# Performance work log

Hardware: AMD Instinct MI355X
Metric: run time of the kernel (lower is better)

The kernel has to match this reference:

```python
import jax, jax.numpy as jnp
import numpy as np

B, S, D = 4, 2048, 768
H = 12
HD = D // H  # 64


def setup_inputs() -> dict:
    key = jax.random.key(0)
    k1, k2, k3 = jax.random.split(key, 3)
    return {
        "hidden_states": jax.random.normal(k1, (B, S, D), dtype=jnp.float32),
        "W_attn": jax.random.normal(k2, (D, 3 * D), dtype=jnp.float32) * 0.02,
        "b_attn": jnp.zeros((3 * D,), dtype=jnp.float32),
        "W_proj": jax.random.normal(k3, (D, D), dtype=jnp.float32) * 0.02,
        "b_proj": jnp.zeros((D,), dtype=jnp.float32),
    }


def reference(hidden_states, W_attn, b_attn, W_proj, b_proj):
    # Conv1D c_attn: x @ W + b -> [B, S, 3D]
    qkv = hidden_states @ W_attn + b_attn
    q, k, v = jnp.split(qkv, 3, axis=-1)

    def split_heads(t):
        # [B, S, D] -> [B, H, S, HD]
        return t.reshape(B, S, H, HD).transpose(0, 2, 1, 3)

    q, k, v = split_heads(q), split_heads(k), split_heads(v)

    # attn_weights = q @ k^T / sqrt(head_dim); NOTE: this module variant applies
    # no causal mask when attention_mask is None (faithful to source _attn).
    scale = jnp.asarray(HD, dtype=q.dtype) ** 0.5
    scores = jnp.einsum("bhqd,bhkd->bhqk", q, k) / scale
    weights = jax.nn.softmax(scores, axis=-1)

    attn = jnp.einsum("bhqk,bhkd->bhqd", weights, v)
    # merge heads -> [B, S, D]
    attn = attn.transpose(0, 2, 1, 3).reshape(B, S, D)
    # Conv1D c_proj
    out = attn @ W_proj + b_proj
    return out
```

## Files before the change

### kernel.cpp

```cpp
#include <hip/hip_runtime.h>

typedef short short8 __attribute__((ext_vector_type(8)));
typedef float f32x2 __attribute__((ext_vector_type(2)));
typedef float f32x4 __attribute__((ext_vector_type(4)));
typedef float f32x16 __attribute__((ext_vector_type(16)));

__device__ __forceinline__ unsigned short f2bf(float f){
  union { float f; unsigned int u; } x; x.f = f;
  unsigned int r = x.u + 0x7fffu + ((x.u >> 16) & 1u);
  return (unsigned short)(r >> 16);
}

__device__ __forceinline__ void gload_lds16(const void* g, void* l){
  __builtin_amdgcn_global_load_lds(
      (const __attribute__((address_space(1))) void*)g,
      (__attribute__((address_space(3))) void*)l, 16, 0, 0);
}

__device__ __forceinline__ unsigned int cvtpk_bf16(float lo, float hi){
  unsigned int r;
  asm("v_cvt_pk_bf16_f32 %0, %1, %2" : "=v"(r) : "v"(lo), "v"(hi));
  return r;
}

__device__ __forceinline__ f32x2 pk_add(f32x2 a, f32x2 b){
  f32x2 d;
  asm("v_pk_add_f32 %0, %1, %2" : "=v"(d) : "v"(a), "v"(b));
  return d;
}

__global__ __launch_bounds__(256) void prep_fused(const float* __restrict__ hs,
                                                  unsigned short* __restrict__ hbf,
                                                  const float* __restrict__ Wa,
                                                  unsigned short* __restrict__ WaT,
                                                  const float* __restrict__ Wp,
                                                  unsigned short* __restrict__ WpT){
  __shared__ float tile[64][68];
  const int b = blockIdx.x;
  const int t = threadIdx.x;
  if (b < 2048){
    const int n4 = 8192 * 768 / 4;
    int i = b * 256 + t;
    for (; i < n4; i += 2048 * 256){
      float4 v = ((const float4*)hs)[i];
      ushort4 o;
      o.x = f2bf(v.x); o.y = f2bf(v.y); o.z = f2bf(v.z); o.w = f2bf(v.w);
      ((ushort4*)hbf)[i] = o;
    }
    return;
  }
  const float* W; unsigned short* WT; int K, N, n0, k0;
  if (b < 2480){
    const int idx = b - 2048;
    W = Wa; WT = WaT; K = 768; N = 2304;
    n0 = (idx % 36) * 64; k0 = (idx / 36) * 64;
  } else {
    const int idx = b - 2480;
    W = Wp; WT = WpT; K = 768; N = 768;
    n0 = (idx % 12) * 64; k0 = (idx / 12) * 64;
  }
  const int qn = (t & 15) * 4;
  #pragma unroll
  for (int i = 0; i < 4; ++i){
    const int kk = (t >> 4) + i * 16;
    float4 v = *(const float4*)&W[(size_t)(k0 + kk) * N + n0 + qn];
    tile[kk][qn + 0] = v.x; tile[kk][qn + 1] = v.y;
    tile[kk][qn + 2] = v.z; tile[kk][qn + 3] = v.w;
  }
  __syncthreads();
  const int qk = (t & 15) * 4;
  #pragma unroll
  for (int i = 0; i < 4; ++i){
    const int nn = (t >> 4) + i * 16;
    ushort4 o;
    o.x = f2bf(tile[qk + 0][nn]); o.y = f2bf(tile[qk + 1][nn]);
    o.z = f2bf(tile[qk + 2][nn]); o.w = f2bf(tile[qk + 3][nn]);
    *(ushort4*)&WT[(size_t)(n0 + nn) * K + k0 + qk] = o;
  }
}

__global__ __launch_bounds__(256) void gemm_qk(const unsigned short* __restrict__ A,
                                               const unsigned short* __restrict__ Bt,
                                               const float* __restrict__ bias,
                                               unsigned short* __restrict__ qkv){
  __shared__ unsigned short As[2][128 * 32];
  __shared__ unsigned short Bs[2][128 * 32];
  const int tid = threadIdx.x;
  const int wave = tid >> 6, lane = tid & 63;
  const int g = lane >> 4, l15 = lane & 15;
  const int wr = wave >> 1, wc = wave & 1;
  const int d = blockIdx.x;
  const int w = (d & 7) * 96 + (d >> 3);
  const int m0 = (w / 12) * 128, n0 = (w % 12) * 128;

  f32x4 acc[4][4] = {};

  auto stage = [&](int bi, int kt){
    const int k0 = kt * 32;
    #pragma unroll
    for (int c = 0; c < 2; ++c){
      const int z = c * 4096 + tid * 16;
      const int r = z >> 6;
      const int ys = (z & 63) ^ ((r & 3) << 4);
      gload_lds16((const char*)A + ((size_t)(m0 + r) * 768 + k0) * 2 + ys,
                  (char*)&As[bi][0] + c * 4096 + wave * 1024);
      gload_lds16((const char*)Bt + ((size_t)(n0 + r) * 768 + k0) * 2 + ys,
                  (char*)&Bs[bi][0] + c * 4096 + wave * 1024);
    }
  };

  stage(0, 0);
  for (int kt = 0; kt < 24; ++kt){
    __syncthreads();
    if (kt + 1 < 24) stage((kt + 1) & 1, kt + 1);
    const char* Ab = (const char*)&As[kt & 1][0];
    const char* Bb = (const char*)&Bs[kt & 1][0];
    short8 a[4], b[4];
    #pragma unroll
    for (int mt = 0; mt < 4; ++mt){
      const int row = wr * 64 + mt * 16 + l15;
      a[mt] = *(const short8*)(Ab + row * 64 + ((g * 16) ^ ((row & 3) << 4)));
    }
    #pragma unroll
    for (int nt = 0; nt < 4; ++nt){
      const int row = wc * 64 + nt * 16 + l15;
      b[nt] = *(const short8*)(Bb + row * 64 + ((g * 16) ^ ((row & 3) << 4)));
    }
    #pragma unroll
    for (int mt = 0; mt < 4; ++mt)
      #pragma unroll
      for (int nt = 0; nt < 4; ++nt)
        acc[mt][nt] = __builtin_amdgcn_mfma_f32_16x16x32_bf16(a[mt], b[nt], acc[mt][nt], 0, 0, 0);
  }

  #pragma unroll
  for (int nt = 0; nt < 4; ++nt){
    const int n = n0 + wc * 64 + nt * 16 + l15;
    const int which = (n >= 768) ? 1 : 0;
    const float bs = bias[n];
    const int h2 = (n - which * 768) >> 6;
    const int hd = n & 63;
    const float sc = (which == 0) ? 0.18033688f : 1.0f;
    #pragma unroll
    for (int mt = 0; mt < 4; ++mt)
      #pragma unroll
      for (int r = 0; r < 4; ++r){
        const int m = m0 + wr * 64 + mt * 16 + 4 * g + r;
        const int bb = m >> 11, sidx = m & 2047;
        qkv[(size_t)which * 6291456u +
            ((((size_t)bb * 12 + h2) * 2048 + sidx) * 64 + hd)] = f2bf((acc[mt][nt][r] + bs) * sc);
      }
  }
}

__global__ __launch_bounds__(256) void gemm_v(const unsigned short* __restrict__ A,
                                              const unsigned short* __restrict__ Bt,
                                              const float* __restrict__ bias,
                                              unsigned short* __restrict__ qkv){
  __shared__ unsigned short As[2][128 * 32];
  __shared__ unsigned short Bs[2][128 * 32];
  const int tid = threadIdx.x;
  const int wave = tid >> 6, lane = tid & 63;
  const int g = lane >> 4, l15 = lane & 15;
  const int wr = wave >> 1, wc = wave & 1;
  const int d = blockIdx.x;
  const int w = (d & 7) * 48 + (d >> 3);
  const int m0 = (w / 6) * 128, n0 = 1536 + (w % 6) * 128;

  f32x4 acc[4][4] = {};

  auto stage = [&](int bi, int kt){
    const int k0 = kt * 32;
    #pragma unroll
    for (int c = 0; c < 2; ++c){
      const int z = c * 4096 + tid * 16;
      const int r = z >> 6;
      const int ys = (z & 63) ^ ((r & 3) << 4);
      gload_lds16((const char*)A + ((size_t)(m0 + r) * 768 + k0) * 2 + ys,
                  (char*)&As[bi][0] + c * 4096 + wave * 1024);
      gload_lds16((const char*)Bt + ((size_t)(n0 + r) * 768 + k0) * 2 + ys,
                  (char*)&Bs[bi][0] + c * 4096 + wave * 1024);
    }
  };

  stage(0, 0);
  for (int kt = 0; kt < 24; ++kt){
    __syncthreads();
    if (kt + 1 < 24) stage((kt + 1) & 1, kt + 1);
    const char* Ab = (const char*)&As[kt & 1][0];
    const char* Bb = (const char*)&Bs[kt & 1][0];
    short8 aw[4], bx[4];
    #pragma unroll
    for (int nt = 0; nt < 4; ++nt){
      const int row = wr * 64 + nt * 16 + l15;
      aw[nt] = *(const short8*)(Bb + row * 64 + ((g * 16) ^ ((row & 3) << 4)));
    }
    #pragma unroll
    for (int mt = 0; mt < 4; ++mt){
      const int row = wc * 64 + mt * 16 + l15;
      bx[mt] = *(const short8*)(Ab + row * 64 + ((g * 16) ^ ((row & 3) << 4)));
    }
    #pragma unroll
    for (int nt = 0; nt < 4; ++nt)
      #pragma unroll
      for (int mt = 0; mt < 4; ++mt)
        acc[nt][mt] = __builtin_amdgcn_mfma_f32_16x16x32_bf16(aw[nt], bx[mt], acc[nt][mt], 0, 0, 0);
  }

  unsigned short* vbase = qkv + (size_t)2 * 6291456;
  const int bb = m0 >> 11;
  #pragma unroll
  for (int nt = 0; nt < 4; ++nt)
    #pragma unroll
    for (int r = 0; r < 4; ++r){
      const int n = n0 + wr * 64 + nt * 16 + 4 * g + r;
      const int hd = n & 63;
      const int head = (n - 1536) >> 6;
      const float bs = bias[n];
      unsigned short* dst = vbase + ((size_t)(bb * 12 + head) * 64 + hd) * 2048;
      #pragma unroll
      for (int mt = 0; mt < 4; ++mt){
        const int m = m0 + wc * 64 + mt * 16 + l15;
        dst[m & 2047] = f2bf(acc[nt][mt][r] + bs);
      }
    }
}

__global__ __launch_bounds__(256) void gemm_proj(const unsigned short* __restrict__ A,
                                                 const unsigned short* __restrict__ Bt,
                                                 const float* __restrict__ bias,
                                                 float* __restrict__ out){
  __shared__ unsigned short As[2][128 * 32];
  __shared__ unsigned short Bs[2][64 * 32];
  const int tid = threadIdx.x;
  const int wave = tid >> 6, lane = tid & 63;
  const int g = lane >> 4, l15 = lane & 15;
  const int d = blockIdx.x;
  const int w = (d & 7) * 96 + (d >> 3);
  const int m0 = (w / 12) * 128, n0 = (w % 12) * 64;

  f32x4 acc[2][4] = {};

  auto stage = [&](int bi, int kt){
    const int k0 = kt * 32;
    #pragma unroll
    for (int c = 0; c < 2; ++c){
      const int z = c * 4096 + tid * 16;
      const int r = z >> 6;
      const int ys = (z & 63) ^ ((r & 3) << 4);
      gload_lds16((const char*)A + ((size_t)(m0 + r) * 768 + k0) * 2 + ys,
                  (char*)&As[bi][0] + c * 4096 + wave * 1024);
    }
    const int z = tid * 16;
    const int r = z >> 6;
    const int ys = (z & 63) ^ ((r & 3) << 4);
    gload_lds16((const char*)Bt + ((size_t)(n0 + r) * 768 + k0) * 2 + ys,
                (char*)&Bs[bi][0] + wave * 1024);
  };

  stage(0, 0);
  for (int kt = 0; kt < 24; ++kt){
    __syncthreads();
    if (kt + 1 < 24) stage((kt + 1) & 1, kt + 1);
    const char* Ab = (const char*)&As[kt & 1][0];
    const char* Bb = (const char*)&Bs[kt & 1][0];
    short8 a[2], b[4];
    #pragma unroll
    for (int mt = 0; mt < 2; ++mt){
      const int row = wave * 32 + mt * 16 + l15;
      a[mt] = *(const short8*)(Ab + row * 64 + ((g * 16) ^ ((row & 3) << 4)));
    }
    #pragma unroll
    for (int nt = 0; nt < 4; ++nt){
      const int row = nt * 16 + l15;
      b[nt] = *(const short8*)(Bb + row * 64 + ((g * 16) ^ ((row & 3) << 4)));
    }
    #pragma unroll
    for (int mt = 0; mt < 2; ++mt)
      #pragma unroll
      for (int nt = 0; nt < 4; ++nt)
        acc[mt][nt] = __builtin_amdgcn_mfma_f32_16x16x32_bf16(a[mt], b[nt], acc[mt][nt], 0, 0, 0);
  }

  #pragma unroll
  for (int mt = 0; mt < 2; ++mt)
    #pragma unroll
    for (int nt = 0; nt < 4; ++nt){
      const int n = n0 + nt * 16 + l15;
      const float bs = bias[n];
      #pragma unroll
      for (int r = 0; r < 4; ++r){
        const int m = m0 + wave * 32 + mt * 16 + 4 * g + r;
        out[(size_t)m * 768 + n] = acc[mt][nt][r] + bs;
      }
    }
}

__global__ __launch_bounds__(256) void attn_fwd12(const unsigned short* __restrict__ qw,
                                                  const unsigned short* __restrict__ kw,
                                                  const unsigned short* __restrict__ vtw,
                                                  unsigned short* __restrict__ aout){
  __shared__ unsigned short Ks[2][64 * 64];
  __shared__ unsigned short Vs[2][64 * 64];
  const int tid = threadIdx.x;
  const int wave = tid >> 6, lane = tid & 63;
  const int h = lane >> 5, ql = lane & 31;
  const int dd = blockIdx.x;
  const int wk = (dd & 7) * 96 + (dd >> 3);
  const int bh = wk >> 4;
  const int q0 = (wk & 15) * 128 + wave * 32;
  const size_t base = (size_t)bh * 2048 * 64;

  short8 qf[4];
  #pragma unroll
  for (int c = 0; c < 4; ++c)
    qf[c] = *(const short8*)(qw + base + (size_t)(q0 + ql) * 64 + c * 16 + h * 8);

  f32x16 acc[2] = {};
  float lsum = 0.f;

  auto stageKV = [&](int bi, int t){
    #pragma unroll
    for (int c = 0; c < 2; ++c){
      const int z = c * 4096 + tid * 16;
      const int r = z >> 7, y = z & 127;
      const int ys = y ^ ((r & 7) << 4);
      gload_lds16((const char*)kw + (base + (size_t)(t * 64 + r) * 64) * 2 + ys,
                  (char*)&Ks[bi][0] + z);
      gload_lds16((const char*)vtw + (base + (size_t)r * 2048 + t * 64) * 2 + ys,
                  (char*)&Vs[bi][0] + z);
    }
  };

  stageKV(0, 0);
  __syncthreads();

  for (int t = 0; t < 32; ++t){
    const int buf = t & 1;
    if (t + 1 < 32) stageKV(buf ^ 1, t + 1);

    f32x16 s[2] = {};
    #pragma unroll
    for (int kt = 0; kt < 2; ++kt)
      #pragma unroll
      for (int c = 0; c < 4; ++c){
        const int row = kt * 32 + ql;
        short8 af = *(const short8*)((const char*)&Ks[buf][0] + row * 128 +
                                     ((c * 32 + h * 16) ^ ((row & 7) << 4)));
        s[kt] = __builtin_amdgcn_mfma_f32_32x32x16_bf16(af, qf[c], s[kt], 0, 0, 0);
      }

    #pragma unroll
    for (int kt = 0; kt < 2; ++kt)
      #pragma unroll
      for (int r = 0; r < 16; ++r)
        s[kt][r] = __builtin_amdgcn_exp2f(s[kt][r]);

    {
      f32x2 a0 = pk_add(__builtin_shufflevector(s[0], s[0], 0, 1),  __builtin_shufflevector(s[0], s[0], 2, 3));
      f32x2 a1 = pk_add(__builtin_shufflevector(s[0], s[0], 4, 5),  __builtin_shufflevector(s[0], s[0], 6, 7));
      f32x2 a2 = pk_add(__builtin_shufflevector(s[0], s[0], 8, 9),  __builtin_shufflevector(s[0], s[0], 10, 11));
      f32x2 a3 = pk_add(__builtin_shufflevector(s[0], s[0], 12, 13), __builtin_shufflevector(s[0], s[0], 14, 15));
      f32x2 b0 = pk_add(__builtin_shufflevector(s[1], s[1], 0, 1),  __builtin_shufflevector(s[1], s[1], 2, 3));
      f32x2 b1 = pk_add(__builtin_shufflevector(s[1], s[1], 4, 5),  __builtin_shufflevector(s[1], s[1], 6, 7));
      f32x2 b2 = pk_add(__builtin_shufflevector(s[1], s[1], 8, 9),  __builtin_shufflevector(s[1], s[1], 10, 11));
      f32x2 b3 = pk_add(__builtin_shufflevector(s[1], s[1], 12, 13), __builtin_shufflevector(s[1], s[1], 14, 15));
      a0 = pk_add(a0, a1); a2 = pk_add(a2, a3);
      b0 = pk_add(b0, b1); b2 = pk_add(b2, b3);
      a0 = pk_add(a0, a2); b0 = pk_add(b0, b2);
      a0 = pk_add(a0, b0);
      lsum += a0[0] + a0[1];
    }

    #pragma unroll
    for (int kt = 0; kt < 2; ++kt){
      unsigned int w0 = cvtpk_bf16(s[kt][0],  s[kt][1]),  x0 = cvtpk_bf16(s[kt][4],  s[kt][5]);
      asm("v_permlane32_swap_b32 %0, %1" : "+v"(w0), "+v"(x0));
      unsigned int w1 = cvtpk_bf16(s[kt][2],  s[kt][3]),  x1 = cvtpk_bf16(s[kt][6],  s[kt][7]);
      asm("v_permlane32_swap_b32 %0, %1" : "+v"(w1), "+v"(x1));
      unsigned int w2 = cvtpk_bf16(s[kt][8],  s[kt][9]),  x2 = cvtpk_bf16(s[kt][12], s[kt][13]);
      asm("v_permlane32_swap_b32 %0, %1" : "+v"(w2), "+v"(x2));
      unsigned int w3 = cvtpk_bf16(s[kt][10], s[kt][11]), x3 = cvtpk_bf16(s[kt][14], s[kt][15]);
      asm("v_permlane32_swap_b32 %0, %1" : "+v"(w3), "+v"(x3));
      union { unsigned int u[4]; short8 v; } pa2[2];
      pa2[0].u[0] = w0; pa2[0].u[1] = w1; pa2[0].u[2] = x0; pa2[0].u[3] = x1;
      pa2[1].u[0] = w2; pa2[1].u[1] = w3; pa2[1].u[2] = x2; pa2[1].u[3] = x3;
      #pragma unroll
      for (int c2 = 0; c2 < 2; ++c2){
        const int kc = kt * 2 + c2;
        #pragma unroll
        for (int ht = 0; ht < 2; ++ht){
          const int row = ht * 32 + ql;
          short8 vb = *(const short8*)((const char*)&Vs[buf][0] + row * 128 +
                                       ((kc * 32 + h * 16) ^ ((row & 7) << 4)));
          acc[ht] = __builtin_amdgcn_mfma_f32_32x32x16_bf16(pa2[c2].v, vb, acc[ht], 0, 0, 0);
        }
      }
    }

    __syncthreads();
  }

  lsum += __shfl_xor(lsum, 32);
  const float inv = 1.0f / lsum;
  const int bb = bh / 12, hh = bh % 12;
  #pragma unroll
  for (int g4 = 0; g4 < 4; ++g4)
    #pragma unroll
    for (int j = 0; j < 4; ++j){
      const int row = 8 * g4 + 4 * h + j;
      const float li = __shfl(inv, row);
      #pragma unroll
      for (int ht = 0; ht < 2; ++ht)
        aout[(size_t)(bb * 2048 + q0 + row) * 768 + hh * 64 + ht * 32 + ql] =
            f2bf(acc[ht][4 * g4 + j] * li);
    }
}

extern "C" void kernel_launch(void* const* d_in, const int* in_sizes, int n_in,
                              void* d_out, int out_size, void* d_ws, size_t ws_size,
                              hipStream_t stream){
  const float* hs = (const float*)d_in[0];
  const float* Wa = (const float*)d_in[1];
  const float* ba = (const float*)d_in[2];
  const float* Wp = (const float*)d_in[3];
  const float* bp = (const float*)d_in[4];

  char* ws = (char*)d_ws;
  unsigned short* hbf = (unsigned short*)ws;
  unsigned short* WaT = (unsigned short*)(ws + 12582912);
  unsigned short* WpT = (unsigned short*)(ws + 12582912 + 3538944);
  unsigned short* qkv = (unsigned short*)(ws + 12582912 + 3538944 + 1179648);
  unsigned short* abf = qkv + (size_t)3 * 6291456;

  prep_fused<<<dim3(2624), dim3(256), 0, stream>>>(hs, hbf, Wa, WaT, Wp, WpT);
  gemm_qk<<<dim3(768), dim3(256), 0, stream>>>(hbf, WaT, ba, qkv);
  gemm_v<<<dim3(384), dim3(256), 0, stream>>>(hbf, WaT, ba, qkv);
  attn_fwd12<<<dim3(768), dim3(256), 0, stream>>>(qkv, qkv + 6291456, qkv + (size_t)2 * 6291456, abf);
  gemm_proj<<<dim3(768), dim3(256), 0, stream>>>(abf, WpT, bp, (float*)d_out);
}
```

Measured before the change: 154.4 us.

## Split attention over two KV halves with a separate combine kernel

Attention is split along the key dimension: each block now handles half of the 2048 keys, giving 1536 blocks instead of 768. Unnormalized partial outputs go to two bf16 buffers along with per-row exp sums, and a new combine kernel adds the partials and normalizes them. The aim is better CU occupancy and less tail effect on the attention kernel. The cost is an extra launch, extra memory traffic for the partials, and a second bf16 rounding of the unnormalized partials. There is no max-subtraction, so adding the partials directly is valid, but accuracy may shift slightly.

```diff
diff --git a/kernel.cpp b/kernel.cpp
--- a/kernel.cpp
+++ b/kernel.cpp
@@ -9,6 +9,11 @@
   union { float f; unsigned int u; } x; x.f = f;
   unsigned int r = x.u + 0x7fffu + ((x.u >> 16) & 1u);
   return (unsigned short)(r >> 16);
+}
+
+__device__ __forceinline__ float bf2f(unsigned short u){
+  union { unsigned int u; float f; } x; x.u = ((unsigned int)u) << 16;
+  return x.f;
 }
 
 __device__ __forceinline__ void gload_lds16(const void* g, void* l){
@@ -296,19 +301,24 @@
     }
 }
 
-__global__ __launch_bounds__(256) void attn_fwd12(const unsigned short* __restrict__ qw,
+__global__ __launch_bounds__(256) void attn_split(const unsigned short* __restrict__ qw,
                                                   const unsigned short* __restrict__ kw,
                                                   const unsigned short* __restrict__ vtw,
-                                                  unsigned short* __restrict__ aout){
+                                                  unsigned short* __restrict__ p0,
+                                                  unsigned short* __restrict__ p1,
+                                                  float* __restrict__ lsums){
   __shared__ unsigned short Ks[2][64 * 64];
   __shared__ unsigned short Vs[2][64 * 64];
   const int tid = threadIdx.x;
   const int wave = tid >> 6, lane = tid & 63;
   const int h = lane >> 5, ql = lane & 31;
   const int dd = blockIdx.x;
-  const int wk = (dd & 7) * 96 + (dd >> 3);
-  const int bh = wk >> 4;
-  const int q0 = (wk & 15) * 128 + wave * 32;
+  const int wk = (dd & 7) * 192 + (dd >> 3);
+  const int bh = wk >> 5;
+  const int sub = wk & 31;
+  const int q0 = (sub >> 1) * 128 + wave * 32;
+  const int half = sub & 1;
+  const int tbeg = half * 16;
   const size_t base = (size_t)bh * 2048 * 64;
 
   short8 qf[4];
@@ -332,12 +342,12 @@
     }
   };
 
-  stageKV(0, 0);
+  stageKV(0, tbeg);
   __syncthreads();
 
-  for (int t = 0; t < 32; ++t){
-    const int buf = t & 1;
-    if (t + 1 < 32) stageKV(buf ^ 1, t + 1);
+  for (int tt = 0; tt < 16; ++tt){
+    const int buf = tt & 1;
+    if (tt + 1 < 16) stageKV(buf ^ 1, tbeg + tt + 1);
 
     f32x16 s[2] = {};
     #pragma unroll
@@ -402,19 +412,38 @@
   }
 
   lsum += __shfl_xor(lsum, 32);
-  const float inv = 1.0f / lsum;
+  if (h == 0) lsums[half * 98304 + bh * 2048 + q0 + ql] = lsum;
+  unsigned short* pO = half ? p1 : p0;
   const int bb = bh / 12, hh = bh % 12;
   #pragma unroll
   for (int g4 = 0; g4 < 4; ++g4)
     #pragma unroll
     for (int j = 0; j < 4; ++j){
       const int row = 8 * g4 + 4 * h + j;
-      const float li = __shfl(inv, row);
       #pragma unroll
       for (int ht = 0; ht < 2; ++ht)
-        aout[(size_t)(bb * 2048 + q0 + row) * 768 + hh * 64 + ht * 32 + ql] =
-            f2bf(acc[ht][4 * g4 + j] * li);
-    }
+        pO[(size_t)(bb * 2048 + q0 + row) * 768 + hh * 64 + ht * 32 + ql] =
+            f2bf(acc[ht][4 * g4 + j]);
+    }
+}
+
+__global__ __launch_bounds__(256) void attn_combine(unsigned short* __restrict__ p0,
+                                                    const unsigned short* __restrict__ p1,
+                                                    const float* __restrict__ lsums){
+  const int i = blockIdx.x * 256 + threadIdx.x;
+  const int e = i * 8;
+  const int col = e % 768;
+  const int row = e / 768;
+  const int bh = (row >> 11) * 12 + (col >> 6);
+  const int sidx = row & 2047;
+  const float inv = 1.0f / (lsums[bh * 2048 + sidx] + lsums[98304 + bh * 2048 + sidx]);
+  short8 a = *(const short8*)(p0 + e);
+  short8 b = *(const short8*)(p1 + e);
+  short8 o;
+  #pragma unroll
+  for (int j = 0; j < 8; ++j)
+    o[j] = (short)f2bf((bf2f((unsigned short)a[j]) + bf2f((unsigned short)b[j])) * inv);
+  *(short8*)(p0 + e) = o;
 }
 
 extern "C" void kernel_launch(void* const* d_in, const int* in_sizes, int n_in,
@@ -433,9 +462,13 @@
   unsigned short* qkv = (unsigned short*)(ws + 12582912 + 3538944 + 1179648);
   unsigned short* abf = qkv + (size_t)3 * 6291456;
 
+  float* lsums = (float*)WaT;
+
   prep_fused<<<dim3(2624), dim3(256), 0, stream>>>(hs, hbf, Wa, WaT, Wp, WpT);
   gemm_qk<<<dim3(768), dim3(256), 0, stream>>>(hbf, WaT, ba, qkv);
   gemm_v<<<dim3(384), dim3(256), 0, stream>>>(hbf, WaT, ba, qkv);
-  attn_fwd12<<<dim3(768), dim3(256), 0, stream>>>(qkv, qkv + 6291456, qkv + (size_t)2 * 6291456, abf);
+  attn_split<<<dim3(1536), dim3(256), 0, stream>>>(qkv, qkv + 6291456, qkv + (size_t)2 * 6291456,
+                                                   abf, hbf, lsums);
+  attn_combine<<<dim3(3072), dim3(256), 0, stream>>>(abf, hbf, lsums);
   gemm_proj<<<dim3(768), dim3(256), 0, stream>>>(abf, WpT, bp, (float*)d_out);
 }
```

Measured after the change: 160.5 us. +3.9%, slower.
